# Kernel tuning notes

Measured on AMD Instinct MI355X. Metric: run time of the kernel, lower is better.

Reference implementation:

```python
import jax, jax.numpy as jnp
import numpy as np

BETA = 0.904837
V_TH = 1.0
SURR_K = 25.0


def _spike(v):
    # Heaviside forward; surrogate gradient irrelevant for fwd-only.
    return (v >= V_TH).astype(v.dtype)


def setup_inputs() -> dict:
    key = jax.random.key(0)
    k1, k2 = jax.random.split(key)
    B, T, H = 16, 1024, 2048
    input_current = jax.random.normal(k1, (B, T, H), dtype=jnp.float32)
    v_init = jax.random.normal(k2, (B, H), dtype=jnp.float32)
    return {"input_current": input_current, "v_init": v_init}


def reference(input_current, v_init):
    # input_current: (B, T, H), v_init: (B, H)
    def step(carry, i_t):
        v, s_prev = carry
        v = BETA * v * (1.0 - s_prev) + i_t  # hard reset via (1 - s_prev)
        s = _spike(v)
        return (v, s), (s, v)

    s0 = jnp.zeros_like(v_init)
    # scan over time axis: move T to leading dim
    (v_final, _), (spikes_t, membrane_t) = jax.lax.scan(
        step, (v_init, s0), jnp.swapaxes(input_current, 0, 1)
    )
    spikes = jnp.swapaxes(spikes_t, 0, 1)      # (B, T, H)
    membrane = jnp.swapaxes(membrane_t, 0, 1)  # (B, T, H)
    return spikes, membrane, v_final
```

## Files before the change

kernel.cpp:

```cpp
#include <hip/hip_runtime.h>


constexpr int B_ = 16;
constexpr int T_ = 1024;
constexpr int H_ = 2048;
constexpr int H2 = H_ / 2;
constexpr float BETA = 0.904837f;
constexpr int D = 16;

typedef __attribute__((ext_vector_type(2))) float fx2;

__global__ __launch_bounds__(64) void lif_fwd_kernel(
    const fx2* __restrict__ in,
    const fx2* __restrict__ v0,
    fx2* __restrict__ sp,
    fx2* __restrict__ mem,
    fx2* __restrict__ vf)
{
    const int idx = blockIdx.x * 64 + threadIdx.x;
    const int b  = idx >> 10;
    const int h2 = idx & (H2 - 1);
    const size_t base = (size_t)b * T_ * H2 + (size_t)h2;

    const fx2* __restrict__ ip = in + base;
    fx2* __restrict__ spp = sp + base;
    fx2* __restrict__ mp  = mem + base;

    fx2 vv = v0[idx];
    float v0r = vv[0], v1r = vv[1];
    float s0r = 0.0f, s1r = 0.0f;

    fx2 buf[D];
#pragma unroll
    for (int j = 0; j < D; ++j)
        buf[j] = __builtin_nontemporal_load(ip + (size_t)j * H2);

    int t0 = 0;
    for (; t0 < T_ - D; t0 += D) {
#pragma unroll
        for (int j = 0; j < D; ++j) {
            const fx2 x = buf[j];
            buf[j] = __builtin_nontemporal_load(ip + (size_t)(t0 + D + j) * H2);

            v0r = BETA * v0r * (1.0f - s0r) + x[0];
            v1r = BETA * v1r * (1.0f - s1r) + x[1];
            s0r = (v0r >= 1.0f) ? 1.0f : 0.0f;
            s1r = (v1r >= 1.0f) ? 1.0f : 0.0f;

            const size_t o = (size_t)(t0 + j) * H2;
            fx2 sv; sv[0] = s0r; sv[1] = s1r;
            fx2 mv; mv[0] = v0r; mv[1] = v1r;
            __builtin_nontemporal_store(sv, spp + o);
            __builtin_nontemporal_store(mv, mp + o);
        }
    }

#pragma unroll
    for (int j = 0; j < D; ++j) {
        const fx2 x = buf[j];
        v0r = BETA * v0r * (1.0f - s0r) + x[0];
        v1r = BETA * v1r * (1.0f - s1r) + x[1];
        s0r = (v0r >= 1.0f) ? 1.0f : 0.0f;
        s1r = (v1r >= 1.0f) ? 1.0f : 0.0f;

        const size_t o = (size_t)(t0 + j) * H2;
        fx2 sv; sv[0] = s0r; sv[1] = s1r;
        fx2 mv; mv[0] = v0r; mv[1] = v1r;
        __builtin_nontemporal_store(sv, spp + o);
        __builtin_nontemporal_store(mv, mp + o);
    }

    fx2 vfv; vfv[0] = v0r; vfv[1] = v1r;
    vf[idx] = vfv;
}

extern "C" void kernel_launch(void* const* d_in, const int* in_sizes, int n_in,
                              void* d_out, int out_size, void* d_ws, size_t ws_size,
                              hipStream_t stream) {
    const fx2* in = (const fx2*)d_in[0];
    const fx2* v0 = (const fx2*)d_in[1];

    float* out = (float*)d_out;
    const size_t n_bth = (size_t)B_ * T_ * H_;
    fx2* sp  = (fx2*)out;
    fx2* mem = (fx2*)(out + n_bth);
    fx2* vf  = (fx2*)(out + 2 * n_bth);

    const int threads = B_ * H2;
    const int block = 64;
    const int grid = threads / block;
    lif_fwd_kernel<<<grid, block, 0, stream>>>(in, v0, sp, mem, vf);
}
```

Baseline: 385.7 us.

## Stage input through double-buffered LDS with async global-to-LDS copies

Replaces the per-thread register prefetch ring of 16 timesteps with a double-buffered LDS staging scheme. `global_load_lds` 16-byte async copies bring in 32-timestep chunks of each block's 64-column tile while the previous chunk is being computed. This raises the number of bytes in flight per wave and frees registers, since the kernel runs only one wave per CU and is latency bound. The cost is 32 KB of LDS per block, a `__syncthreads` per chunk, and correctness that depends on the compiler inserting the right wait counts for the LDS-DMA loads before the barrier.

```diff
diff --git a/kernel.cpp b/kernel.cpp
--- a/kernel.cpp
+++ b/kernel.cpp
@@ -6,79 +6,93 @@
 constexpr int H_ = 2048;
 constexpr int H2 = H_ / 2;
 constexpr float BETA = 0.904837f;
-constexpr int D = 16;
+constexpr int C  = 32;
+constexpr int NCH = T_ / C;
+constexpr int PAIRS = C / 2;
 
 typedef __attribute__((ext_vector_type(2))) float fx2;
 
+__device__ __forceinline__ void async_copy16(const void* g, void* s) {
+    __builtin_amdgcn_global_load_lds(
+        (const __attribute__((address_space(1))) void*)g,
+        (__attribute__((address_space(3))) void*)s,
+        16, 0, 0);
+}
+
 __global__ __launch_bounds__(64) void lif_fwd_kernel(
-    const fx2* __restrict__ in,
-    const fx2* __restrict__ v0,
+    const float* __restrict__ in,
+    const float* __restrict__ v0,
     fx2* __restrict__ sp,
     fx2* __restrict__ mem,
     fx2* __restrict__ vf)
 {
-    const int idx = blockIdx.x * 64 + threadIdx.x;
-    const int b  = idx >> 10;
-    const int h2 = idx & (H2 - 1);
-    const size_t base = (size_t)b * T_ * H2 + (size_t)h2;
+    __shared__ fx2 lds_buf[2][C * 64];
 
-    const fx2* __restrict__ ip = in + base;
-    fx2* __restrict__ spp = sp + base;
-    fx2* __restrict__ mp  = mem + base;
+    const int lane = threadIdx.x;
+    const int w    = blockIdx.x;
+    const int b    = w >> 4;
+    const int colb = (w & 15) * 64;
 
-    fx2 vv = v0[idx];
+    const size_t seq_base = (size_t)b * T_ * H2 + colb;
+
+    const int sel = lane >> 5;
+    const char* stage_base = (const char*)in + seq_base * 8
+                           + (size_t)sel * (H2 * 8)
+                           + (size_t)(lane & 31) * 16;
+
+    fx2* __restrict__ spp = sp  + seq_base + lane;
+    fx2* __restrict__ mpp = mem + seq_base + lane;
+
+    const int vidx = b * H2 + colb + lane;
+    const fx2 vv = ((const fx2*)v0)[vidx];
     float v0r = vv[0], v1r = vv[1];
     float s0r = 0.0f, s1r = 0.0f;
 
-    fx2 buf[D];
 #pragma unroll
-    for (int j = 0; j < D; ++j)
-        buf[j] = __builtin_nontemporal_load(ip + (size_t)j * H2);
+    for (int p = 0; p < PAIRS; ++p)
+        async_copy16(stage_base + (size_t)(2 * p) * (H2 * 8),
+                     &lds_buf[0][p * 128]);
 
-    int t0 = 0;
-    for (; t0 < T_ - D; t0 += D) {
+    for (int c = 0; c < NCH; ++c) {
+        __syncthreads();
+
+        if (c + 1 < NCH) {
+            const char* gb = stage_base + (size_t)(c + 1) * C * (H2 * 8);
+            const int nb = (c + 1) & 1;
 #pragma unroll
-        for (int j = 0; j < D; ++j) {
-            const fx2 x = buf[j];
-            buf[j] = __builtin_nontemporal_load(ip + (size_t)(t0 + D + j) * H2);
+            for (int p = 0; p < PAIRS; ++p)
+                async_copy16(gb + (size_t)(2 * p) * (H2 * 8),
+                             &lds_buf[nb][p * 128]);
+        }
+
+        const fx2* lbuf = lds_buf[c & 1];
+        const size_t obase = (size_t)c * C * H2;
+#pragma unroll
+        for (int s = 0; s < C; ++s) {
+            const fx2 x = lbuf[s * 64 + lane];
 
             v0r = BETA * v0r * (1.0f - s0r) + x[0];
             v1r = BETA * v1r * (1.0f - s1r) + x[1];
             s0r = (v0r >= 1.0f) ? 1.0f : 0.0f;
             s1r = (v1r >= 1.0f) ? 1.0f : 0.0f;
 
-            const size_t o = (size_t)(t0 + j) * H2;
+            const size_t o = obase + (size_t)s * H2;
             fx2 sv; sv[0] = s0r; sv[1] = s1r;
             fx2 mv; mv[0] = v0r; mv[1] = v1r;
             __builtin_nontemporal_store(sv, spp + o);
-            __builtin_nontemporal_store(mv, mp + o);
+            __builtin_nontemporal_store(mv, mpp + o);
         }
     }
 
-#pragma unroll
-    for (int j = 0; j < D; ++j) {
-        const fx2 x = buf[j];
-        v0r = BETA * v0r * (1.0f - s0r) + x[0];
-        v1r = BETA * v1r * (1.0f - s1r) + x[1];
-        s0r = (v0r >= 1.0f) ? 1.0f : 0.0f;
-        s1r = (v1r >= 1.0f) ? 1.0f : 0.0f;
-
-        const size_t o = (size_t)(t0 + j) * H2;
-        fx2 sv; sv[0] = s0r; sv[1] = s1r;
-        fx2 mv; mv[0] = v0r; mv[1] = v1r;
-        __builtin_nontemporal_store(sv, spp + o);
-        __builtin_nontemporal_store(mv, mp + o);
-    }
-
     fx2 vfv; vfv[0] = v0r; vfv[1] = v1r;
-    vf[idx] = vfv;
+    vf[vidx] = vfv;
 }
 
 extern "C" void kernel_launch(void* const* d_in, const int* in_sizes, int n_in,
                               void* d_out, int out_size, void* d_ws, size_t ws_size,
                               hipStream_t stream) {
-    const fx2* in = (const fx2*)d_in[0];
-    const fx2* v0 = (const fx2*)d_in[1];
+    const float* in = (const float*)d_in[0];
+    const float* v0 = (const float*)d_in[1];
 
     float* out = (float*)d_out;
     const size_t n_bth = (size_t)B_ * T_ * H_;
@@ -86,8 +100,6 @@
     fx2* mem = (fx2*)(out + n_bth);
     fx2* vf  = (fx2*)(out + 2 * n_bth);
 
-    const int threads = B_ * H2;
-    const int block = 64;
-    const int grid = threads / block;
-    lif_fwd_kernel<<<grid, block, 0, stream>>>(in, v0, sp, mem, vf);
+    const int grid = B_ * (H2 / 64);
+    lif_fwd_kernel<<<grid, 64, 0, stream>>>(in, v0, sp, mem, vf);
 }
```

Result: faster. 357.2 us (-7.4%).
